# Optimization experiments

Hardware: AMD Instinct MI355X
Metric: run time of the kernel (lower is better)

Reference implementation:

```python
import jax, jax.numpy as jnp
import numpy as np

N_NODES = 50000
N_EDGES = 800000
IN_CH = 64
HID = 128


def setup_inputs() -> dict:
    key = jax.random.key(0)
    ks = jax.random.split(key, 8)
    s = 0.05
    x = jax.random.normal(ks[0], (N_NODES, IN_CH), dtype=jnp.float32)
    edge_index = jax.random.randint(ks[1], (2, N_EDGES), 0, N_NODES, dtype=jnp.int64)
    return {
        "x": x,
        "edge_index": edge_index,
        "W1l": jax.random.normal(ks[2], (HID, IN_CH), dtype=jnp.float32) * s,
        "b1l": jnp.zeros((HID,), dtype=jnp.float32),
        "W1r": jax.random.normal(ks[3], (HID, IN_CH), dtype=jnp.float32) * s,
        "W2l": jax.random.normal(ks[4], (HID, HID), dtype=jnp.float32) * s,
        "b2l": jnp.zeros((HID,), dtype=jnp.float32),
        "W2r": jax.random.normal(ks[5], (HID, HID), dtype=jnp.float32) * s,
        "Wrec": jax.random.normal(ks[6], (IN_CH, HID), dtype=jnp.float32) * s,
        "brec": jnp.zeros((IN_CH,), dtype=jnp.float32),
    }


def _sage_conv(x, src, dst, Wl, bl, Wr, n_nodes):
    # mean aggregation of source features at destination nodes
    msg_sum = jax.ops.segment_sum(x[src], dst, num_segments=n_nodes)  # [N, d]
    deg = jax.ops.segment_sum(jnp.ones((src.shape[0],), x.dtype), dst,
                              num_segments=n_nodes)  # [N]
    mean = msg_sum / jnp.maximum(deg, 1.0)[:, None]
    # SAGEConv: lin_l(aggr) + lin_r(x_i); lin_l has bias, lin_r does not
    return mean @ Wl.T + bl + x @ Wr.T


def reference(x, edge_index, W1l, b1l, W1r, W2l, b2l, W2r, Wrec, brec):
    src, dst = edge_index[0], edge_index[1]
    n = x.shape[0]
    h = _sage_conv(x, src, dst, W1l, b1l, W1r, n)
    h = jax.nn.relu(h)  # activation between layers, none after last
    z = _sage_conv(h, src, dst, W2l, b2l, W2r, n)
    x_recon = z @ Wrec.T + brec
    return (z, x_recon)
```

## Files before the change

kernel.cpp:

```cpp
#include <hip/hip_runtime.h>

#define N_NODES 50000
#define N_EDGES 800000
#define IN_CH 64
#define HID 128
#define NB_SCAN ((N_NODES + 255) / 256)

typedef short short8 __attribute__((ext_vector_type(8)));
typedef float f32x4 __attribute__((ext_vector_type(4)));

static __device__ __forceinline__ unsigned short f2bf(float f) {
    unsigned u = __float_as_uint(f);
    u += 0x7FFF + ((u >> 16) & 1);
    return (unsigned short)(u >> 16);
}
static __device__ __forceinline__ float bflo(unsigned v) { return __uint_as_float(v << 16); }
static __device__ __forceinline__ float bfhi(unsigned v) { return __uint_as_float(v & 0xFFFF0000u); }


__global__ __launch_bounds__(256) void k_cvt(const float* __restrict__ src,
                                             unsigned short* __restrict__ dst, int n4) {
    int i = blockIdx.x * 256 + threadIdx.x;
    if (i < n4) {
        float4 v = ((const float4*)src)[i];
        unsigned lo = f2bf(v.x) | ((unsigned)f2bf(v.y) << 16);
        unsigned hi = f2bf(v.z) | ((unsigned)f2bf(v.w) << 16);
        ((uint2*)dst)[i] = make_uint2(lo, hi);
    }
}

__global__ __launch_bounds__(256) void k_cvt_w(const float* __restrict__ W1l, const float* __restrict__ W1r,
                                               const float* __restrict__ W2l, const float* __restrict__ W2r,
                                               const float* __restrict__ Wrec, unsigned short* __restrict__ dst) {
    int i = blockIdx.x * 256 + threadIdx.x;
    int e = i * 4;
    if (e >= 57344) return;
    const float* src; int off;
    if (e < 8192)       { src = W1l;  off = 0; }
    else if (e < 16384) { src = W1r;  off = 8192; }
    else if (e < 32768) { src = W2l;  off = 16384; }
    else if (e < 49152) { src = W2r;  off = 32768; }
    else                { src = Wrec; off = 49152; }
    float4 v = *(const float4*)(src + (e - off));
    unsigned lo = f2bf(v.x) | ((unsigned)f2bf(v.y) << 16);
    unsigned hi = f2bf(v.z) | ((unsigned)f2bf(v.w) << 16);
    *(uint2*)(dst + e) = make_uint2(lo, hi);
}


__global__ __launch_bounds__(256) void k_deg(const int* __restrict__ ei, int* __restrict__ deg) {
    int e = blockIdx.x * 256 + threadIdx.x;
    if (e < N_EDGES) {
        int d = ei[N_EDGES + e];
        if ((unsigned)d < N_NODES) atomicAdd(&deg[d], 1);
    }
}

__global__ __launch_bounds__(256) void k_scan1(const int* __restrict__ deg,
                                               int* __restrict__ excl,
                                               int* __restrict__ bsum) {
    int gid = blockIdx.x * 256 + threadIdx.x;
    int v = (gid < N_NODES) ? deg[gid] : 0;
    int lane = threadIdx.x & 63, wv = threadIdx.x >> 6;
    int s = v;
    #pragma unroll
    for (int d = 1; d < 64; d <<= 1) {
        int t = __shfl_up(s, d);
        if (lane >= d) s += t;
    }
    __shared__ int wsum[4];
    if (lane == 63) wsum[wv] = s;
    __syncthreads();
    int add = 0;
    #pragma unroll
    for (int w = 0; w < 4; w++) add += (w < wv) ? wsum[w] : 0;
    s += add;
    if (gid < N_NODES) excl[gid] = s - v;
    if (threadIdx.x == 255) bsum[blockIdx.x] = s;
}

__global__ __launch_bounds__(256) void k_scan2(const int* __restrict__ bsum,
                                               int* __restrict__ bpre,
                                               int* __restrict__ offs) {
    int tid = threadIdx.x;
    int v = (tid < NB_SCAN) ? bsum[tid] : 0;
    int lane = tid & 63, wv = tid >> 6;
    int s = v;
    #pragma unroll
    for (int d = 1; d < 64; d <<= 1) {
        int t = __shfl_up(s, d);
        if (lane >= d) s += t;
    }
    __shared__ int wsum[4];
    if (lane == 63) wsum[wv] = s;
    __syncthreads();
    int add = 0;
    #pragma unroll
    for (int w = 0; w < 4; w++) add += (w < wv) ? wsum[w] : 0;
    s += add;
    if (tid < NB_SCAN) bpre[tid] = s - v;
    if (tid == NB_SCAN - 1) offs[N_NODES] = s;
}

__global__ __launch_bounds__(256) void k_scan3(const int* __restrict__ excl,
                                               const int* __restrict__ bpre,
                                               int* __restrict__ offs) {
    int gid = blockIdx.x * 256 + threadIdx.x;
    if (gid < N_NODES) offs[gid] = excl[gid] + bpre[blockIdx.x];
}

__global__ __launch_bounds__(256) void k_fill(const int* __restrict__ ei, const int* __restrict__ offs,
                                              int* __restrict__ cursor, int* __restrict__ csr) {
    int e = blockIdx.x * 256 + threadIdx.x;
    if (e < N_EDGES) {
        int s = ei[e];
        int d = ei[N_EDGES + e];
        if ((unsigned)d < N_NODES && (unsigned)s < N_NODES) {
            int pos = atomicAdd(&cursor[d], 1);
            csr[offs[d] + pos] = s;
        }
    }
}


template <int CH>
__global__ __launch_bounds__(256) void k_agg_cs(const unsigned short* __restrict__ X,
                                                const int* __restrict__ csr,
                                                const int* __restrict__ offs,
                                                unsigned short* __restrict__ out,
                                                int c0) {
    int wid = (blockIdx.x * 256 + threadIdx.x) >> 6;
    int lane = threadIdx.x & 63;
    if (wid >= N_NODES) return;
    int beg = offs[wid], end = offs[wid + 1];
    int degn = end - beg;
    float inv = 1.0f / (float)(degn > 0 ? degn : 1);
    int g = lane >> 4, hl = lane & 15;
    float sx = 0.f, sy = 0.f;
    for (int e = beg + g; e < end; e += 4) {
        int idx = __builtin_nontemporal_load(&csr[e]);
        unsigned v = *(const unsigned*)(X + (size_t)idx * CH + c0 + hl * 2);
        sx += bflo(v); sy += bfhi(v);
    }
    sx += __shfl_xor(sx, 16); sy += __shfl_xor(sy, 16);
    sx += __shfl_xor(sx, 32); sy += __shfl_xor(sy, 32);
    if (g == 0) {
        unsigned o = f2bf(sx * inv) | ((unsigned)f2bf(sy * inv) << 16);
        *(unsigned*)(out + (size_t)wid * CH + c0 + hl * 2) = o;
    }
}


template <int NOUT, int K1, bool DUAL, bool RELU, bool WF32, bool WBF16>
__global__ __launch_bounds__(256) void k_gemm_mfma(const unsigned short* __restrict__ A0,
                                                   const unsigned short* __restrict__ A1,
                                                   const unsigned short* __restrict__ W0,
                                                   const unsigned short* __restrict__ W1,
                                                   const float* __restrict__ bias,
                                                   float* __restrict__ out,
                                                   unsigned short* __restrict__ outb) {
    constexpr int NF = NOUT / 16;
    constexpr int NPH = DUAL ? 2 : 1;
    __shared__ char wlds[NOUT * K1 * 2];
    int tid = threadIdx.x;
    int lane = tid & 63;
    int wv = tid >> 6;
    int m0 = blockIdx.x * 64 + wv * 16;
    int col16 = lane & 15;
    int kg = lane >> 4;
    int arow = m0 + col16;
    if (arow >= N_NODES) arow = N_NODES - 1;

    f32x4 acc[NF] = {};

    #pragma unroll
    for (int ph = 0; ph < NPH; ph++) {
        const unsigned short* Wp = ph ? W1 : W0;
        const unsigned short* Ap = ph ? A1 : A0;
        if (ph) __syncthreads();
        constexpr int CHUNKS = NOUT * K1 / 8;
        #pragma unroll
        for (int it = 0; it < CHUNKS / 256; it++) {
            int ci = tid + it * 256;
            int j = ci / (K1 / 8);
            int c = (ci % (K1 / 8)) * 8;
            short8 w = *(const short8*)(Wp + (size_t)j * K1 + c);
            int byte = ((j * K1 + c) * 2) ^ ((j & 7) << 4);
            *(short8*)(wlds + byte) = w;
        }
        __syncthreads();
        #pragma unroll
        for (int ks = 0; ks < K1 / 32; ks++) {
            int kk = ks * 32;
            short8 a = *(const short8*)(Ap + (size_t)arow * K1 + kk + kg * 8);
            #pragma unroll
            for (int j = 0; j < NF; j++) {
                int row = j * 16 + col16;
                int byte = ((row * K1 + kk + kg * 8) * 2) ^ ((row & 7) << 4);
                short8 b = *(const short8*)(wlds + byte);
                acc[j] = __builtin_amdgcn_mfma_f32_16x16x32_bf16(a, b, acc[j], 0, 0, 0);
            }
        }
    }

    int col = lane & 15;
    int r0 = (lane >> 4) * 4;
    #pragma unroll
    for (int j = 0; j < NF; j++) {
        float bv = bias[j * 16 + col];
        #pragma unroll
        for (int r = 0; r < 4; r++) {
            int grow = m0 + r0 + r;
            if (grow < N_NODES) {
                float v = acc[j][r] + bv;
                if (RELU) v = fmaxf(v, 0.f);
                if (WF32)  out[(size_t)grow * NOUT + j * 16 + col] = v;
                if (WBF16) outb[(size_t)grow * NOUT + j * 16 + col] = f2bf(v);
            }
        }
    }
}


extern "C" void kernel_launch(void* const* d_in, const int* in_sizes, int n_in,
                              void* d_out, int out_size, void* d_ws, size_t ws_size,
                              hipStream_t stream) {
    const float* x    = (const float*)d_in[0];
    const int*   ei   = (const int*)d_in[1];
    const float* W1l  = (const float*)d_in[2];
    const float* b1l  = (const float*)d_in[3];
    const float* W1r  = (const float*)d_in[4];
    const float* W2l  = (const float*)d_in[5];
    const float* b2l  = (const float*)d_in[6];
    const float* W2r  = (const float*)d_in[7];
    const float* Wrec = (const float*)d_in[8];
    const float* brec = (const float*)d_in[9];

    float* z    = (float*)d_out;
    float* xrec = (float*)d_out + (size_t)N_NODES * HID;

    char* ws = (char*)d_ws;
    int*   deg    = (int*)(ws);
    int*   offs   = (int*)(ws + (256u << 10));
    int*   cursor = (int*)(ws + (512u << 10));
    int*   excl   = (int*)(ws + (768u << 10));
    int*   bsum   = (int*)(ws + (1024u << 10));
    int*   bpre   = (int*)(ws + (1028u << 10));
    int*   csr    = (int*)(ws + (2u << 20));
    unsigned short* wb     = (unsigned short*)(ws + (5632u << 10));
    unsigned short* xb     = (unsigned short*)(ws + (6u  << 20));
    unsigned short* mean1b = (unsigned short*)(ws + (13u << 20));
    unsigned short* mean2b = (unsigned short*)(ws + (13u << 20));
    unsigned short* hb     = (unsigned short*)(ws + (26u << 20));
    unsigned short* zb     = (unsigned short*)(ws + (39u << 20));

    unsigned short* W1lb  = wb;
    unsigned short* W1rb  = wb + 8192;
    unsigned short* W2lb  = wb + 16384;
    unsigned short* W2rb  = wb + 32768;
    unsigned short* Wrecb = wb + 49152;

    (void)hipMemsetAsync(deg, 0, N_NODES * sizeof(int), stream);
    (void)hipMemsetAsync(cursor, 0, N_NODES * sizeof(int), stream);

    int egrid = (N_EDGES + 255) / 256;
    int ngrid = (N_NODES + 63) / 64;
    int agrid = N_NODES / 4;

    k_cvt_w<<<56, 256, 0, stream>>>(W1l, W1r, W2l, W2r, Wrec, wb);
    k_cvt<<<(800000 + 255) / 256, 256, 0, stream>>>(x, xb, 800000);

    k_deg<<<egrid, 256, 0, stream>>>(ei, deg);
    k_scan1<<<NB_SCAN, 256, 0, stream>>>(deg, excl, bsum);
    k_scan2<<<1, 256, 0, stream>>>(bsum, bpre, offs);
    k_scan3<<<NB_SCAN, 256, 0, stream>>>(excl, bpre, offs);
    k_fill<<<egrid, 256, 0, stream>>>(ei, offs, cursor, csr);

    for (int c = 0; c < 64; c += 32)
        k_agg_cs<64><<<agrid, 256, 0, stream>>>(xb, csr, offs, mean1b, c);
    k_gemm_mfma<128, 64, true, true, false, true>
        <<<ngrid, 256, 0, stream>>>(mean1b, xb, W1lb, W1rb, b1l, nullptr, hb);
    for (int c = 0; c < 128; c += 32)
        k_agg_cs<128><<<agrid, 256, 0, stream>>>(hb, csr, offs, mean2b, c);
    k_gemm_mfma<128, 128, true, false, true, true>
        <<<ngrid, 256, 0, stream>>>(mean2b, hb, W2lb, W2rb, b2l, z, zb);
    k_gemm_mfma<64, 128, false, false, true, false>
        <<<ngrid, 256, 0, stream>>>(zb, nullptr, Wrecb, nullptr, brec, xrec, nullptr);
}
```

Measured before the change: 406.7 us.

## Aggregate full feature rows per wave instead of channel-sliced passes

Replaces the channel-sliced aggregation (two launches for 64 channels, four for 128) with a single launch per layer. Each wave now gathers whole bf16 rows, using 32 lanes × 2 edges for 64 channels and 64 lanes with a 2-edge unroll for 128 channels. This cuts repeated CSR index reads and kernel launches, and reads full 128/256-byte rows per neighbor instead of 64-byte slices. In exchange there is less edge-level parallelism per wave, so more gather latency is serialized for high-degree nodes.

```diff
diff --git a/kernel.cpp b/kernel.cpp
--- a/kernel.cpp
+++ b/kernel.cpp
@@ -122,32 +122,58 @@
     }
 }
 
-
-template <int CH>
-__global__ __launch_bounds__(256) void k_agg_cs(const unsigned short* __restrict__ X,
+__global__ __launch_bounds__(256) void k_agg64b(const unsigned short* __restrict__ X,
                                                 const int* __restrict__ csr,
                                                 const int* __restrict__ offs,
-                                                unsigned short* __restrict__ out,
-                                                int c0) {
+                                                unsigned short* __restrict__ out) {
     int wid = (blockIdx.x * 256 + threadIdx.x) >> 6;
     int lane = threadIdx.x & 63;
     if (wid >= N_NODES) return;
     int beg = offs[wid], end = offs[wid + 1];
     int degn = end - beg;
     float inv = 1.0f / (float)(degn > 0 ? degn : 1);
-    int g = lane >> 4, hl = lane & 15;
+    int half = lane >> 5, hl = lane & 31;
     float sx = 0.f, sy = 0.f;
-    for (int e = beg + g; e < end; e += 4) {
+    for (int e = beg + half; e < end; e += 2) {
         int idx = __builtin_nontemporal_load(&csr[e]);
-        unsigned v = *(const unsigned*)(X + (size_t)idx * CH + c0 + hl * 2);
+        unsigned v = *(const unsigned*)(X + (size_t)idx * 64 + hl * 2);
         sx += bflo(v); sy += bfhi(v);
     }
-    sx += __shfl_xor(sx, 16); sy += __shfl_xor(sy, 16);
-    sx += __shfl_xor(sx, 32); sy += __shfl_xor(sy, 32);
-    if (g == 0) {
+    sx += __shfl_xor(sx, 32);
+    sy += __shfl_xor(sy, 32);
+    if (half == 0) {
         unsigned o = f2bf(sx * inv) | ((unsigned)f2bf(sy * inv) << 16);
-        *(unsigned*)(out + (size_t)wid * CH + c0 + hl * 2) = o;
-    }
+        *(unsigned*)(out + (size_t)wid * 64 + hl * 2) = o;
+    }
+}
+
+__global__ __launch_bounds__(256) void k_agg128b(const unsigned short* __restrict__ X,
+                                                 const int* __restrict__ csr,
+                                                 const int* __restrict__ offs,
+                                                 unsigned short* __restrict__ out) {
+    int wid = (blockIdx.x * 256 + threadIdx.x) >> 6;
+    int lane = threadIdx.x & 63;
+    if (wid >= N_NODES) return;
+    int beg = offs[wid], end = offs[wid + 1];
+    int degn = end - beg;
+    float inv = 1.0f / (float)(degn > 0 ? degn : 1);
+    float sx = 0.f, sy = 0.f;
+    int e = beg;
+    for (; e + 2 <= end; e += 2) {
+        int i0 = __builtin_nontemporal_load(&csr[e]);
+        int i1 = __builtin_nontemporal_load(&csr[e + 1]);
+        unsigned a = *(const unsigned*)(X + (size_t)i0 * 128 + lane * 2);
+        unsigned b = *(const unsigned*)(X + (size_t)i1 * 128 + lane * 2);
+        sx += bflo(a) + bflo(b);
+        sy += bfhi(a) + bfhi(b);
+    }
+    if (e < end) {
+        int i0 = __builtin_nontemporal_load(&csr[e]);
+        unsigned a = *(const unsigned*)(X + (size_t)i0 * 128 + lane * 2);
+        sx += bflo(a); sy += bfhi(a);
+    }
+    unsigned o = f2bf(sx * inv) | ((unsigned)f2bf(sy * inv) << 16);
+    *(unsigned*)(out + (size_t)wid * 128 + lane * 2) = o;
 }
 
 
@@ -265,7 +291,7 @@
 
     int egrid = (N_EDGES + 255) / 256;
     int ngrid = (N_NODES + 63) / 64;
-    int agrid = N_NODES / 4;
+    int agrid = (N_NODES + 3) / 4;
 
     k_cvt_w<<<56, 256, 0, stream>>>(W1l, W1r, W2l, W2r, Wrec, wb);
     k_cvt<<<(800000 + 255) / 256, 256, 0, stream>>>(x, xb, 800000);
@@ -276,12 +302,10 @@
     k_scan3<<<NB_SCAN, 256, 0, stream>>>(excl, bpre, offs);
     k_fill<<<egrid, 256, 0, stream>>>(ei, offs, cursor, csr);
 
-    for (int c = 0; c < 64; c += 32)
-        k_agg_cs<64><<<agrid, 256, 0, stream>>>(xb, csr, offs, mean1b, c);
+    k_agg64b<<<agrid, 256, 0, stream>>>(xb, csr, offs, mean1b);
     k_gemm_mfma<128, 64, true, true, false, true>
         <<<ngrid, 256, 0, stream>>>(mean1b, xb, W1lb, W1rb, b1l, nullptr, hb);
-    for (int c = 0; c < 128; c += 32)
-        k_agg_cs<128><<<agrid, 256, 0, stream>>>(hb, csr, offs, mean2b, c);
+    k_agg128b<<<agrid, 256, 0, stream>>>(hb, csr, offs, mean2b);
     k_gemm_mfma<128, 128, true, false, true, true>
         <<<ngrid, 256, 0, stream>>>(mean2b, hb, W2lb, W2rb, b2l, z, zb);
     k_gemm_mfma<64, 128, false, false, true, false>
```

Result: faster. 330.2 us (-18.8%).
